# Performance work log

Measured on AMD Instinct MI355X. Metric: run time of the kernel, lower is better.

The kernel has to match this reference:

```python
import jax, jax.numpy as jnp
import numpy as np

N_NODES = 50000
N_EDGES = 800000
IN_C = 128
OUT_C = 128
ALPHA = 0.2  # leaky_relu negative slope (args.egat_alpha)
EDGE_K = 3   # edgefeat width, fixed by W_out in-dim = 3*out_channels


def setup_inputs() -> dict:
    key = jax.random.key(0)
    k = jax.random.split(key, 7)
    h = jax.random.normal(k[0], (N_NODES, IN_C), dtype=jnp.float32)
    edge_index = jax.random.randint(k[1], (2, N_EDGES), 0, N_NODES, dtype=jnp.int64)
    edgefeat = jax.random.uniform(k[2], (N_EDGES, EDGE_K), dtype=jnp.float32)
    # glorot-initialized linear weights (stored as [in, out] for x @ W)
    def glorot(kk, fan_in, fan_out):
        lim = jnp.sqrt(6.0 / (fan_in + fan_out)).astype(jnp.float32)
        return jax.random.uniform(kk, (fan_in, fan_out), jnp.float32, -lim, lim)
    W = glorot(k[3], IN_C, OUT_C)
    a1 = glorot(k[4], OUT_C, 1)
    a2 = glorot(k[5], OUT_C, 1)
    W_out = glorot(k[6], EDGE_K * OUT_C, OUT_C)
    return {"h": h, "edge_index": edge_index, "edgefeat": edgefeat,
            "W": W, "a1": a1, "a2": a2, "W_out": W_out}


def reference(h, edge_index, edgefeat, W, a1, a2, W_out):
    src = edge_index[0]  # j: message source
    dst = edge_index[1]  # i: aggregation target
    n = h.shape[0]

    Wh = h @ W                                   # [N, C]
    s1 = Wh @ a1                                 # [N, 1] alpha_j scores
    s2 = Wh @ a2                                 # [N, 1] alpha_i scores

    # edge_update: leaky_relu(alpha_j + alpha_i) * edge_attr, then edge softmax over dst
    e = s1[src] + s2[dst]                        # [E, 1]
    e = jnp.where(e >= 0, e, ALPHA * e)
    alpha = e * edgefeat                         # [E, 3]
    m = jax.ops.segment_max(alpha, dst, num_segments=n)      # [N, 3]
    m = jnp.where(jnp.isfinite(m), m, 0.0)
    ex = jnp.exp(alpha - m[dst])
    denom = jax.ops.segment_sum(ex, dst, num_segments=n)     # [N, 3]
    att = ex / (denom[dst] + 1e-16)              # [E, 3] (dropout p applied at eval -> identity)

    # message: outer product att[E,3] x x_j[E,C] -> [E, 3C] -> W_out -> [E, C]
    x_j = Wh[src]                                # [E, C]
    msg = (att[:, :, None] * x_j[:, None, :]).reshape(att.shape[0], EDGE_K * Wh.shape[1])
    msg = msg @ W_out                            # [E, C]

    # aggregate: sum at destination nodes
    out = jax.ops.segment_sum(msg, dst, num_segments=n)      # [N, C]
    return out
```

## Files before the change

### kernel.cpp

```cpp
#include <hip/hip_runtime.h>
#include <hip/hip_bf16.h>

#define ALPHA 0.2f
typedef unsigned int uint32;
typedef __attribute__((ext_vector_type(8))) short short8;
typedef __attribute__((ext_vector_type(4))) float f32x4;

static __device__ __forceinline__ unsigned short f2bf(float f) {
    unsigned int u = __float_as_uint(f);
    u += 0x7fffu + ((u >> 16) & 1u);
    return (unsigned short)(u >> 16);
}
static __device__ __forceinline__ uint32 pk2bf(float lo, float hi) {
    return (uint32)f2bf(lo) | ((uint32)f2bf(hi) << 16);
}
static __device__ __forceinline__ float bflo(uint32 u) { return __uint_as_float(u << 16); }
static __device__ __forceinline__ float bfhi(uint32 u) { return __uint_as_float(u & 0xffff0000u); }

__global__ __launch_bounds__(256) void k1_hist_prep(const int* __restrict__ ei,
                                                    int* __restrict__ counts,
                                                    int* __restrict__ eslot, int E,
                                                    const float* __restrict__ W,
                                                    const float* __restrict__ Wout,
                                                    const float* __restrict__ a1,
                                                    const float* __restrict__ a2,
                                                    unsigned short* __restrict__ WT2,
                                                    float* __restrict__ w1f,
                                                    float* __restrict__ w2f, int nbh) {
    __shared__ float Wos[128 * 16];
    const int tid = threadIdx.x;
    if ((int)blockIdx.x < nbh) {
        int e = blockIdx.x * 256 + tid;
        if (e < E) eslot[e] = atomicAdd(&counts[ei[E + e]], 1);
        return;
    }
    int bp = blockIdx.x - nbh;
    if (bp < 24) {
        int s = bp >> 3, nb = bp & 7;
        for (int i = tid; i < 2048; i += 256) {
            int c = i >> 4, q = i & 15;
            Wos[i] = Wout[(size_t)(s * 128 + c) * 128 + nb * 16 + q];
        }
        __syncthreads();
        int j = tid & 127, nh = tid >> 7;
        float acc[8];
#pragma unroll
        for (int p = 0; p < 8; ++p) acc[p] = 0.f;
        for (int c = 0; c < 128; ++c) {
            float w = W[j * 128 + c];
#pragma unroll
            for (int p = 0; p < 8; ++p) acc[p] += w * Wos[c * 16 + nh * 8 + p];
        }
#pragma unroll
        for (int p = 0; p < 8; ++p) {
            int n = nb * 16 + nh * 8 + p;
            WT2[((size_t)s * 128 + n) * 128 + j] = f2bf(acc[p]);
        }
    } else {
        if (tid < 128) {
            float acc1 = 0.f, acc2 = 0.f;
            for (int c = 0; c < 128; ++c) {
                float w = W[tid * 128 + c];
                acc1 += w * a1[c];
                acc2 += w * a2[c];
            }
            w1f[tid] = acc1;
            w2f[tid] = acc2;
        }
    }
}

__global__ __launch_bounds__(256) void k2_mmy_scan(const float* __restrict__ h,
                                                   const unsigned short* __restrict__ WT2,
                                                   const float* __restrict__ w1f,
                                                   const float* __restrict__ w2f,
                                                   unsigned short* __restrict__ Yb,
                                                   float* __restrict__ s1,
                                                   float* __restrict__ s2, int M,
                                                   const int* __restrict__ counts,
                                                   int* __restrict__ rowptr,
                                                   int N, int E, int nbm) {
    __shared__ unsigned short As[64 * 128];
    __shared__ unsigned short Bs[128 * 128];
    __shared__ float ws1[128], ws2[128];
    __shared__ int wsums[4];
    __shared__ int base_s;
    const int tid = threadIdx.x;

    if ((int)blockIdx.x >= nbm) {
        const int bs   = blockIdx.x - nbm;
        const int lane = tid & 63, wv = tid >> 6;
        const int limit = bs * 1024;
        int acc = 0;
        for (int i = tid * 4; i < limit; i += 1024) {
            int4 v = *(const int4*)(counts + i);
            acc += v.x + v.y + v.z + v.w;
        }
#pragma unroll
        for (int off = 32; off > 0; off >>= 1) acc += __shfl_down(acc, off);
        if (lane == 0) wsums[wv] = acc;
        __syncthreads();
        if (tid == 0) base_s = wsums[0] + wsums[1] + wsums[2] + wsums[3];
        __syncthreads();
        int i0 = bs * 1024 + tid * 4;
        int v0 = 0, v1 = 0, v2 = 0, v3 = 0;
        if (i0 + 3 < N) {
            int4 v = *(const int4*)(counts + i0);
            v0 = v.x; v1 = v.y; v2 = v.z; v3 = v.w;
        } else {
            if (i0 + 0 < N) v0 = counts[i0 + 0];
            if (i0 + 1 < N) v1 = counts[i0 + 1];
            if (i0 + 2 < N) v2 = counts[i0 + 2];
            if (i0 + 3 < N) v3 = counts[i0 + 3];
        }
        int tt = v0 + v1 + v2 + v3;
        int incl = tt;
#pragma unroll
        for (int off = 1; off < 64; off <<= 1) {
            int t = __shfl_up(incl, off);
            if (lane >= off) incl += t;
        }
        __syncthreads();
        if (lane == 63) wsums[wv] = incl;
        __syncthreads();
        int woff = 0;
        for (int w2 = 0; w2 < wv; ++w2) woff += wsums[w2];
        int base = base_s + woff + (incl - tt);
        if (i0 + 0 < N) rowptr[i0 + 0] = base;
        if (i0 + 1 < N) rowptr[i0 + 1] = base + v0;
        if (i0 + 2 < N) rowptr[i0 + 2] = base + v0 + v1;
        if (i0 + 3 < N) rowptr[i0 + 3] = base + v0 + v1 + v2;
        if (bs == 0 && tid == 0) rowptr[N] = E;
        return;
    }

    const int lane = tid & 63;
    const int w    = tid >> 6;
    const int row0 = blockIdx.x * 64;

    if (tid < 128) ws1[tid] = w1f[tid];
    else           ws2[tid - 128] = w2f[tid - 128];
    __syncthreads();

    const float4* h4 = (const float4*)h;
    float sp1[4], sp2[4];
#pragma unroll
    for (int m = 0; m < 4; ++m) { sp1[m] = 0.f; sp2[m] = 0.f; }
#pragma unroll
    for (int m = 0; m < 4; ++m) {
        int i = m * 256 + tid;
        int r = i >> 4, g = i & 15;
        int rg = row0 + r;
        float4 va = make_float4(0.f, 0.f, 0.f, 0.f), vb = va;
        if (rg < M) {
            va = h4[(size_t)rg * 32 + g * 2];
            vb = h4[(size_t)rg * 32 + g * 2 + 1];
        }
        float4 wa1 = *(const float4*)(ws1 + g * 8);
        float4 wb1 = *(const float4*)(ws1 + g * 8 + 4);
        float4 wa2 = *(const float4*)(ws2 + g * 8);
        float4 wb2 = *(const float4*)(ws2 + g * 8 + 4);
        sp1[m] += va.x * wa1.x + va.y * wa1.y + va.z * wa1.z + va.w * wa1.w
                + vb.x * wb1.x + vb.y * wb1.y + vb.z * wb1.z + vb.w * wb1.w;
        sp2[m] += va.x * wa2.x + va.y * wa2.y + va.z * wa2.z + va.w * wa2.w
                + vb.x * wb2.x + vb.y * wb2.y + vb.z * wb2.z + vb.w * wb2.w;
        uint4 u;
        u.x = pk2bf(va.x, va.y); u.y = pk2bf(va.z, va.w);
        u.z = pk2bf(vb.x, vb.y); u.w = pk2bf(vb.z, vb.w);
        *(uint4*)(As + r * 128 + ((g ^ (r & 15)) * 8)) = u;
    }
#pragma unroll
    for (int m = 0; m < 4; ++m) {
#pragma unroll
        for (int off = 1; off < 16; off <<= 1) {
            sp1[m] += __shfl_xor(sp1[m], off);
            sp2[m] += __shfl_xor(sp2[m], off);
        }
    }
    if ((tid & 15) == 0) {
#pragma unroll
        for (int m = 0; m < 4; ++m) {
            int rg = row0 + m * 16 + (tid >> 4);
            if (rg < M) { s1[rg] = sp1[m]; s2[rg] = sp2[m]; }
        }
    }

    const int ml   = lane & 15;
    const int quad = lane >> 4;
    for (int ks = 0; ks < 3; ++ks) {
        __syncthreads();
#pragma unroll
        for (int m = 0; m < 8; ++m) {
            int i = m * 256 + tid;
            int n = i >> 4, g = i & 15;
            uint4 v = *(const uint4*)(WT2 + (size_t)ks * 16384 + n * 128 + g * 8);
            *(uint4*)(Bs + n * 128 + ((g ^ (n & 15)) * 8)) = v;
        }
        __syncthreads();

        f32x4 acc[8];
#pragma unroll
        for (int nt = 0; nt < 8; ++nt) acc[nt] = (f32x4){0.f, 0.f, 0.f, 0.f};
#pragma unroll
        for (int kc = 0; kc < 4; ++kc) {
            int gl = ((kc * 4 + quad) ^ ml) * 8;
            short8 af = *(const short8*)(As + (w * 16 + ml) * 128 + gl);
#pragma unroll
            for (int nt = 0; nt < 8; ++nt) {
                short8 bf = *(const short8*)(Bs + (nt * 16 + ml) * 128 + gl);
                acc[nt] = __builtin_amdgcn_mfma_f32_16x16x32_bf16(af, bf, acc[nt], 0, 0, 0);
            }
        }
        __syncthreads();
        unsigned short* Ct = Bs;
        int lrow = w * 16 + quad * 4;
#pragma unroll
        for (int r = 0; r < 4; ++r)
#pragma unroll
            for (int nt = 0; nt < 8; ++nt)
                Ct[(lrow + r) * 136 + nt * 16 + ml] = f2bf(acc[nt][r]);
        __syncthreads();
#pragma unroll
        for (int m = 0; m < 4; ++m) {
            int i = m * 256 + tid;
            int r2 = i >> 4, g = i & 15;
            int rg = row0 + r2;
            uint4 v = *(const uint4*)(Ct + r2 * 136 + g * 8);
            if (rg < M)
                *(uint4*)(Yb + (size_t)rg * 384 + ks * 128 + g * 8) = v;
        }
    }
}

__global__ __launch_bounds__(256) void scatter_kernel(const int* __restrict__ ei,
                                                      const float* __restrict__ ef,
                                                      const float* __restrict__ s1,
                                                      const float* __restrict__ s2,
                                                      const int* __restrict__ rowptr,
                                                      const int* __restrict__ eslot,
                                                      uint2* __restrict__ rec8, int E) {
    int e = blockIdx.x * blockDim.x + threadIdx.x;
    if (e >= E) return;
    int src = ei[e];
    int dst = ei[E + e];
    float s = s1[src] + s2[dst];
    s = (s >= 0.f) ? s : ALPHA * s;
    unsigned short b0 = f2bf(__expf(s * ef[e * 3 + 0]));
    unsigned short b1 = f2bf(__expf(s * ef[e * 3 + 1]));
    unsigned short b2 = f2bf(__expf(s * ef[e * 3 + 2]));
    uint2 rv;
    rv.x = (uint32)src | ((uint32)(b0 & 0x7fffu) << 17);
    rv.y = (uint32)(b1 & 0x7fffu) | ((uint32)(b2 & 0x7fffu) << 15);
    int pos = rowptr[dst] + eslot[e];
    rec8[pos] = rv;
}

__global__ __launch_bounds__(256) void agg_kernel(const uint2* __restrict__ rec8,
                                                  const int* __restrict__ rowptr,
                                                  const uint32* __restrict__ Yu,
                                                  float* __restrict__ out, int N) {
    int node = (blockIdx.x * blockDim.x + threadIdx.x) >> 6;
    int lane = threadIdx.x & 63;
    if (node >= N) return;
    int beg = rowptr[node], end = rowptr[node + 1];

    float d0 = 0.f, d1 = 0.f, d2 = 0.f;
    for (int jb = beg + lane; jb < end; jb += 64) {
        uint2 r = rec8[jb];
        d0 += __uint_as_float((r.x >> 1) & 0x7fff0000u);
        d1 += __uint_as_float((r.y << 16) & 0x7fff0000u);
        d2 += __uint_as_float((r.y << 1) & 0x7fff0000u);
    }
#pragma unroll
    for (int off = 32; off > 0; off >>= 1) {
        d0 += __shfl_xor(d0, off);
        d1 += __shfl_xor(d1, off);
        d2 += __shfl_xor(d2, off);
    }
    float inv0 = 1.f / (d0 + 1e-16f);
    float inv1 = 1.f / (d1 + 1e-16f);
    float inv2 = 1.f / (d2 + 1e-16f);

    float a0 = 0.f, a1 = 0.f;
    int j = beg;
    for (; j + 3 < end; j += 4) {
        uint2 r0 = rec8[j], r1 = rec8[j + 1], r2 = rec8[j + 2], r3 = rec8[j + 3];
        const uint32* p0 = Yu + (size_t)(r0.x & 0x1ffffu) * 192;
        const uint32* p1 = Yu + (size_t)(r1.x & 0x1ffffu) * 192;
        const uint32* p2 = Yu + (size_t)(r2.x & 0x1ffffu) * 192;
        const uint32* p3 = Yu + (size_t)(r3.x & 0x1ffffu) * 192;
        uint32 u00 = p0[lane], u01 = p0[64 + lane], u02 = p0[128 + lane];
        uint32 u10 = p1[lane], u11 = p1[64 + lane], u12 = p1[128 + lane];
        uint32 u20 = p2[lane], u21 = p2[64 + lane], u22 = p2[128 + lane];
        uint32 u30 = p3[lane], u31 = p3[64 + lane], u32 = p3[128 + lane];
        float w00 = __uint_as_float((r0.x >> 1) & 0x7fff0000u) * inv0;
        float w01 = __uint_as_float((r0.y << 16) & 0x7fff0000u) * inv1;
        float w02 = __uint_as_float((r0.y << 1) & 0x7fff0000u) * inv2;
        float w10 = __uint_as_float((r1.x >> 1) & 0x7fff0000u) * inv0;
        float w11 = __uint_as_float((r1.y << 16) & 0x7fff0000u) * inv1;
        float w12 = __uint_as_float((r1.y << 1) & 0x7fff0000u) * inv2;
        float w20 = __uint_as_float((r2.x >> 1) & 0x7fff0000u) * inv0;
        float w21 = __uint_as_float((r2.y << 16) & 0x7fff0000u) * inv1;
        float w22 = __uint_as_float((r2.y << 1) & 0x7fff0000u) * inv2;
        float w30 = __uint_as_float((r3.x >> 1) & 0x7fff0000u) * inv0;
        float w31 = __uint_as_float((r3.y << 16) & 0x7fff0000u) * inv1;
        float w32 = __uint_as_float((r3.y << 1) & 0x7fff0000u) * inv2;
        a0 += w00 * bflo(u00) + w01 * bflo(u01) + w02 * bflo(u02);
        a1 += w00 * bfhi(u00) + w01 * bfhi(u01) + w02 * bfhi(u02);
        a0 += w10 * bflo(u10) + w11 * bflo(u11) + w12 * bflo(u12);
        a1 += w10 * bfhi(u10) + w11 * bfhi(u11) + w12 * bfhi(u12);
        a0 += w20 * bflo(u20) + w21 * bflo(u21) + w22 * bflo(u22);
        a1 += w20 * bfhi(u20) + w21 * bfhi(u21) + w22 * bfhi(u22);
        a0 += w30 * bflo(u30) + w31 * bflo(u31) + w32 * bflo(u32);
        a1 += w30 * bfhi(u30) + w31 * bfhi(u31) + w32 * bfhi(u32);
    }
    for (; j < end; ++j) {
        uint2 r0 = rec8[j];
        const uint32* p0 = Yu + (size_t)(r0.x & 0x1ffffu) * 192;
        uint32 u00 = p0[lane], u01 = p0[64 + lane], u02 = p0[128 + lane];
        float w00 = __uint_as_float((r0.x >> 1) & 0x7fff0000u) * inv0;
        float w01 = __uint_as_float((r0.y << 16) & 0x7fff0000u) * inv1;
        float w02 = __uint_as_float((r0.y << 1) & 0x7fff0000u) * inv2;
        a0 += w00 * bflo(u00) + w01 * bflo(u01) + w02 * bflo(u02);
        a1 += w00 * bfhi(u00) + w01 * bfhi(u01) + w02 * bfhi(u02);
    }
    ((float2*)(out + (size_t)node * 128))[lane] = make_float2(a0, a1);
}

extern "C" void kernel_launch(void* const* d_in, const int* in_sizes, int n_in,
                              void* d_out, int out_size, void* d_ws, size_t ws_size,
                              hipStream_t stream) {
    const float* h    = (const float*)d_in[0];
    const int*   ei   = (const int*)d_in[1];
    const float* ef   = (const float*)d_in[2];
    const float* W    = (const float*)d_in[3];
    const float* a1   = (const float*)d_in[4];
    const float* a2   = (const float*)d_in[5];
    const float* Wout = (const float*)d_in[6];
    float*       out  = (float*)d_out;

    const int N = in_sizes[0] / 128;
    const int E = in_sizes[2] / 3;
    const int nchunk = (N + 1023) / 1024;
    const int nbh    = (E + 255) / 256;
    const int nbm    = (N + 63) / 64;

    uint2* rec8 = (uint2*)d_ws;
    unsigned short* Yb  = (unsigned short*)(rec8 + E);
    unsigned short* WT2 = Yb + (size_t)N * 384;
    float* w1f  = (float*)(WT2 + 3 * 128 * 128);
    float* w2f  = w1f + 128;
    float* s1   = w2f + 128;
    float* s2   = s1 + N;
    int* counts = (int*)(s2 + N);
    int* rowptr = counts + N;
    int* eslot  = rowptr + N + 1;

    (void)hipMemsetAsync(counts, 0, (size_t)N * sizeof(int), stream);

    k1_hist_prep<<<nbh + 25, 256, 0, stream>>>(ei, counts, eslot, E,
                                               W, Wout, a1, a2, WT2, w1f, w2f, nbh);
    k2_mmy_scan<<<nbm + nchunk, 256, 0, stream>>>(h, WT2, w1f, w2f, Yb, s1, s2, N,
                                                  counts, rowptr, N, E, nbm);
    scatter_kernel<<<(E + 255) / 256, 256, 0, stream>>>(ei, ef, s1, s2, rowptr, eslot, rec8, E);
    agg_kernel<<<(N * 64 + 255) / 256, 256, 0, stream>>>(rec8, rowptr, (const uint32*)Yb, out, N);
}
```

Before: 248.7 us.

## Aggregate Wh first then apply W_out in a separate GEMM

The algebra is reordered. Instead of precomputing Y = Wh·W_out per node (three 128-wide slices) and gathering 384 bf16 values per edge, the aggregation now gathers only the 128-wide Wh row per edge. It accumulates three attention-weighted sums per node, normalises them, and stores a bf16 z[N,384]. A new MFMA GEMM kernel then multiplies z by W_out^T to produce the output. This cuts per-edge gather traffic threefold and the first GEMM's work, at the cost of an extra kernel launch, an N×384 intermediate round trip, and extra bf16 rounding of z. The workspace is reordered so counts/eslot alias the z buffer.

Result: faster. 223.5 us (-10.1%).

```diff
diff --git a/kernel.cpp b/kernel.cpp
--- a/kernel.cpp
+++ b/kernel.cpp
@@ -24,10 +24,10 @@
                                                     const float* __restrict__ Wout,
                                                     const float* __restrict__ a1,
                                                     const float* __restrict__ a2,
-                                                    unsigned short* __restrict__ WT2,
+                                                    unsigned short* __restrict__ WBT,
+                                                    unsigned short* __restrict__ WoutT,
                                                     float* __restrict__ w1f,
                                                     float* __restrict__ w2f, int nbh) {
-    __shared__ float Wos[128 * 16];
     const int tid = threadIdx.x;
     if ((int)blockIdx.x < nbh) {
         int e = blockIdx.x * 256 + tid;
@@ -35,27 +35,15 @@
         return;
     }
     int bp = blockIdx.x - nbh;
-    if (bp < 24) {
-        int s = bp >> 3, nb = bp & 7;
-        for (int i = tid; i < 2048; i += 256) {
-            int c = i >> 4, q = i & 15;
-            Wos[i] = Wout[(size_t)(s * 128 + c) * 128 + nb * 16 + q];
-        }
-        __syncthreads();
-        int j = tid & 127, nh = tid >> 7;
-        float acc[8];
-#pragma unroll
-        for (int p = 0; p < 8; ++p) acc[p] = 0.f;
-        for (int c = 0; c < 128; ++c) {
-            float w = W[j * 128 + c];
-#pragma unroll
-            for (int p = 0; p < 8; ++p) acc[p] += w * Wos[c * 16 + nh * 8 + p];
-        }
-#pragma unroll
-        for (int p = 0; p < 8; ++p) {
-            int n = nb * 16 + nh * 8 + p;
-            WT2[((size_t)s * 128 + n) * 128 + j] = f2bf(acc[p]);
-        }
+    if (bp < 8) {
+        for (int n = bp * 16; n < bp * 16 + 16; ++n)
+            for (int c = tid; c < 128; c += 256)
+                WBT[n * 128 + c] = f2bf(W[c * 128 + n]);
+    } else if (bp < 24) {
+        int q = bp - 8;
+        for (int n = q * 8; n < q * 8 + 8; ++n)
+            for (int c = tid; c < 384; c += 256)
+                WoutT[n * 384 + c] = f2bf(Wout[c * 128 + n]);
     } else {
         if (tid < 128) {
             float acc1 = 0.f, acc2 = 0.f;
@@ -71,10 +59,10 @@
 }
 
 __global__ __launch_bounds__(256) void k2_mmy_scan(const float* __restrict__ h,
-                                                   const unsigned short* __restrict__ WT2,
+                                                   const unsigned short* __restrict__ WBT,
                                                    const float* __restrict__ w1f,
                                                    const float* __restrict__ w2f,
-                                                   unsigned short* __restrict__ Yb,
+                                                   unsigned short* __restrict__ Whb,
                                                    float* __restrict__ s1,
                                                    float* __restrict__ s2, int M,
                                                    const int* __restrict__ counts,
@@ -185,50 +173,47 @@
         }
     }
 
+#pragma unroll
+    for (int m = 0; m < 8; ++m) {
+        int i = m * 256 + tid;
+        int n = i >> 4, g = i & 15;
+        uint4 v = *(const uint4*)(WBT + n * 128 + g * 8);
+        *(uint4*)(Bs + n * 128 + ((g ^ (n & 15)) * 8)) = v;
+    }
+    __syncthreads();
+
     const int ml   = lane & 15;
     const int quad = lane >> 4;
-    for (int ks = 0; ks < 3; ++ks) {
-        __syncthreads();
-#pragma unroll
-        for (int m = 0; m < 8; ++m) {
-            int i = m * 256 + tid;
-            int n = i >> 4, g = i & 15;
-            uint4 v = *(const uint4*)(WT2 + (size_t)ks * 16384 + n * 128 + g * 8);
-            *(uint4*)(Bs + n * 128 + ((g ^ (n & 15)) * 8)) = v;
-        }
-        __syncthreads();
-
-        f32x4 acc[8];
-#pragma unroll
-        for (int nt = 0; nt < 8; ++nt) acc[nt] = (f32x4){0.f, 0.f, 0.f, 0.f};
-#pragma unroll
-        for (int kc = 0; kc < 4; ++kc) {
-            int gl = ((kc * 4 + quad) ^ ml) * 8;
-            short8 af = *(const short8*)(As + (w * 16 + ml) * 128 + gl);
-#pragma unroll
-            for (int nt = 0; nt < 8; ++nt) {
-                short8 bf = *(const short8*)(Bs + (nt * 16 + ml) * 128 + gl);
-                acc[nt] = __builtin_amdgcn_mfma_f32_16x16x32_bf16(af, bf, acc[nt], 0, 0, 0);
-            }
-        }
-        __syncthreads();
-        unsigned short* Ct = Bs;
-        int lrow = w * 16 + quad * 4;
-#pragma unroll
-        for (int r = 0; r < 4; ++r)
-#pragma unroll
-            for (int nt = 0; nt < 8; ++nt)
-                Ct[(lrow + r) * 136 + nt * 16 + ml] = f2bf(acc[nt][r]);
-        __syncthreads();
-#pragma unroll
-        for (int m = 0; m < 4; ++m) {
-            int i = m * 256 + tid;
-            int r2 = i >> 4, g = i & 15;
-            int rg = row0 + r2;
-            uint4 v = *(const uint4*)(Ct + r2 * 136 + g * 8);
-            if (rg < M)
-                *(uint4*)(Yb + (size_t)rg * 384 + ks * 128 + g * 8) = v;
-        }
+    f32x4 acc[8];
+#pragma unroll
+    for (int nt = 0; nt < 8; ++nt) acc[nt] = (f32x4){0.f, 0.f, 0.f, 0.f};
+#pragma unroll
+    for (int kc = 0; kc < 4; ++kc) {
+        int gl = ((kc * 4 + quad) ^ ml) * 8;
+        short8 af = *(const short8*)(As + (w * 16 + ml) * 128 + gl);
+#pragma unroll
+        for (int nt = 0; nt < 8; ++nt) {
+            short8 bf = *(const short8*)(Bs + (nt * 16 + ml) * 128 + gl);
+            acc[nt] = __builtin_amdgcn_mfma_f32_16x16x32_bf16(af, bf, acc[nt], 0, 0, 0);
+        }
+    }
+    __syncthreads();
+    unsigned short* Ct = Bs;
+    int lrow = w * 16 + quad * 4;
+#pragma unroll
+    for (int r = 0; r < 4; ++r)
+#pragma unroll
+        for (int nt = 0; nt < 8; ++nt)
+            Ct[(lrow + r) * 136 + nt * 16 + ml] = f2bf(acc[nt][r]);
+    __syncthreads();
+#pragma unroll
+    for (int m = 0; m < 4; ++m) {
+        int i = m * 256 + tid;
+        int r2 = i >> 4, g = i & 15;
+        int rg = row0 + r2;
+        uint4 v = *(const uint4*)(Ct + r2 * 136 + g * 8);
+        if (rg < M)
+            *(uint4*)(Whb + (size_t)rg * 128 + g * 8) = v;
     }
 }
 
@@ -258,73 +243,130 @@
 __global__ __launch_bounds__(256) void agg_kernel(const uint2* __restrict__ rec8,
                                                   const int* __restrict__ rowptr,
                                                   const uint32* __restrict__ Yu,
-                                                  float* __restrict__ out, int N) {
+                                                  uint32* __restrict__ zo, int N) {
     int node = (blockIdx.x * blockDim.x + threadIdx.x) >> 6;
     int lane = threadIdx.x & 63;
     if (node >= N) return;
     int beg = rowptr[node], end = rowptr[node + 1];
 
     float d0 = 0.f, d1 = 0.f, d2 = 0.f;
-    for (int jb = beg + lane; jb < end; jb += 64) {
-        uint2 r = rec8[jb];
-        d0 += __uint_as_float((r.x >> 1) & 0x7fff0000u);
-        d1 += __uint_as_float((r.y << 16) & 0x7fff0000u);
-        d2 += __uint_as_float((r.y << 1) & 0x7fff0000u);
-    }
-#pragma unroll
-    for (int off = 32; off > 0; off >>= 1) {
-        d0 += __shfl_xor(d0, off);
-        d1 += __shfl_xor(d1, off);
-        d2 += __shfl_xor(d2, off);
-    }
-    float inv0 = 1.f / (d0 + 1e-16f);
-    float inv1 = 1.f / (d1 + 1e-16f);
-    float inv2 = 1.f / (d2 + 1e-16f);
-
-    float a0 = 0.f, a1 = 0.f;
+    float z0l = 0.f, z0h = 0.f, z1l = 0.f, z1h = 0.f, z2l = 0.f, z2h = 0.f;
     int j = beg;
     for (; j + 3 < end; j += 4) {
         uint2 r0 = rec8[j], r1 = rec8[j + 1], r2 = rec8[j + 2], r3 = rec8[j + 3];
-        const uint32* p0 = Yu + (size_t)(r0.x & 0x1ffffu) * 192;
-        const uint32* p1 = Yu + (size_t)(r1.x & 0x1ffffu) * 192;
-        const uint32* p2 = Yu + (size_t)(r2.x & 0x1ffffu) * 192;
-        const uint32* p3 = Yu + (size_t)(r3.x & 0x1ffffu) * 192;
-        uint32 u00 = p0[lane], u01 = p0[64 + lane], u02 = p0[128 + lane];
-        uint32 u10 = p1[lane], u11 = p1[64 + lane], u12 = p1[128 + lane];
-        uint32 u20 = p2[lane], u21 = p2[64 + lane], u22 = p2[128 + lane];
-        uint32 u30 = p3[lane], u31 = p3[64 + lane], u32 = p3[128 + lane];
-        float w00 = __uint_as_float((r0.x >> 1) & 0x7fff0000u) * inv0;
-        float w01 = __uint_as_float((r0.y << 16) & 0x7fff0000u) * inv1;
-        float w02 = __uint_as_float((r0.y << 1) & 0x7fff0000u) * inv2;
-        float w10 = __uint_as_float((r1.x >> 1) & 0x7fff0000u) * inv0;
-        float w11 = __uint_as_float((r1.y << 16) & 0x7fff0000u) * inv1;
-        float w12 = __uint_as_float((r1.y << 1) & 0x7fff0000u) * inv2;
-        float w20 = __uint_as_float((r2.x >> 1) & 0x7fff0000u) * inv0;
-        float w21 = __uint_as_float((r2.y << 16) & 0x7fff0000u) * inv1;
-        float w22 = __uint_as_float((r2.y << 1) & 0x7fff0000u) * inv2;
-        float w30 = __uint_as_float((r3.x >> 1) & 0x7fff0000u) * inv0;
-        float w31 = __uint_as_float((r3.y << 16) & 0x7fff0000u) * inv1;
-        float w32 = __uint_as_float((r3.y << 1) & 0x7fff0000u) * inv2;
-        a0 += w00 * bflo(u00) + w01 * bflo(u01) + w02 * bflo(u02);
-        a1 += w00 * bfhi(u00) + w01 * bfhi(u01) + w02 * bfhi(u02);
-        a0 += w10 * bflo(u10) + w11 * bflo(u11) + w12 * bflo(u12);
-        a1 += w10 * bfhi(u10) + w11 * bfhi(u11) + w12 * bfhi(u12);
-        a0 += w20 * bflo(u20) + w21 * bflo(u21) + w22 * bflo(u22);
-        a1 += w20 * bfhi(u20) + w21 * bfhi(u21) + w22 * bfhi(u22);
-        a0 += w30 * bflo(u30) + w31 * bflo(u31) + w32 * bflo(u32);
-        a1 += w30 * bfhi(u30) + w31 * bfhi(u31) + w32 * bfhi(u32);
+        uint32 u0 = Yu[(size_t)(r0.x & 0x1ffffu) * 64 + lane];
+        uint32 u1 = Yu[(size_t)(r1.x & 0x1ffffu) * 64 + lane];
+        uint32 u2 = Yu[(size_t)(r2.x & 0x1ffffu) * 64 + lane];
+        uint32 u3 = Yu[(size_t)(r3.x & 0x1ffffu) * 64 + lane];
+        float w00 = __uint_as_float((r0.x >> 1) & 0x7fff0000u);
+        float w01 = __uint_as_float((r0.y << 16) & 0x7fff0000u);
+        float w02 = __uint_as_float((r0.y << 1) & 0x7fff0000u);
+        float w10 = __uint_as_float((r1.x >> 1) & 0x7fff0000u);
+        float w11 = __uint_as_float((r1.y << 16) & 0x7fff0000u);
+        float w12 = __uint_as_float((r1.y << 1) & 0x7fff0000u);
+        float w20 = __uint_as_float((r2.x >> 1) & 0x7fff0000u);
+        float w21 = __uint_as_float((r2.y << 16) & 0x7fff0000u);
+        float w22 = __uint_as_float((r2.y << 1) & 0x7fff0000u);
+        float w30 = __uint_as_float((r3.x >> 1) & 0x7fff0000u);
+        float w31 = __uint_as_float((r3.y << 16) & 0x7fff0000u);
+        float w32 = __uint_as_float((r3.y << 1) & 0x7fff0000u);
+        d0 += w00 + w10 + w20 + w30;
+        d1 += w01 + w11 + w21 + w31;
+        d2 += w02 + w12 + w22 + w32;
+        float y0l = bflo(u0), y0h = bfhi(u0);
+        float y1l = bflo(u1), y1h = bfhi(u1);
+        float y2l = bflo(u2), y2h = bfhi(u2);
+        float y3l = bflo(u3), y3h = bfhi(u3);
+        z0l += w00 * y0l + w10 * y1l + w20 * y2l + w30 * y3l;
+        z0h += w00 * y0h + w10 * y1h + w20 * y2h + w30 * y3h;
+        z1l += w01 * y0l + w11 * y1l + w21 * y2l + w31 * y3l;
+        z1h += w01 * y0h + w11 * y1h + w21 * y2h + w31 * y3h;
+        z2l += w02 * y0l + w12 * y1l + w22 * y2l + w32 * y3l;
+        z2h += w02 * y0h + w12 * y1h + w22 * y2h + w32 * y3h;
     }
     for (; j < end; ++j) {
         uint2 r0 = rec8[j];
-        const uint32* p0 = Yu + (size_t)(r0.x & 0x1ffffu) * 192;
-        uint32 u00 = p0[lane], u01 = p0[64 + lane], u02 = p0[128 + lane];
-        float w00 = __uint_as_float((r0.x >> 1) & 0x7fff0000u) * inv0;
-        float w01 = __uint_as_float((r0.y << 16) & 0x7fff0000u) * inv1;
-        float w02 = __uint_as_float((r0.y << 1) & 0x7fff0000u) * inv2;
-        a0 += w00 * bflo(u00) + w01 * bflo(u01) + w02 * bflo(u02);
-        a1 += w00 * bfhi(u00) + w01 * bfhi(u01) + w02 * bfhi(u02);
-    }
-    ((float2*)(out + (size_t)node * 128))[lane] = make_float2(a0, a1);
+        uint32 u0 = Yu[(size_t)(r0.x & 0x1ffffu) * 64 + lane];
+        float w00 = __uint_as_float((r0.x >> 1) & 0x7fff0000u);
+        float w01 = __uint_as_float((r0.y << 16) & 0x7fff0000u);
+        float w02 = __uint_as_float((r0.y << 1) & 0x7fff0000u);
+        d0 += w00; d1 += w01; d2 += w02;
+        float y0l = bflo(u0), y0h = bfhi(u0);
+        z0l += w00 * y0l; z0h += w00 * y0h;
+        z1l += w01 * y0l; z1h += w01 * y0h;
+        z2l += w02 * y0l; z2h += w02 * y0h;
+    }
+    float i0 = 1.f / (d0 + 1e-16f);
+    float i1 = 1.f / (d1 + 1e-16f);
+    float i2 = 1.f / (d2 + 1e-16f);
+    size_t zb = (size_t)node * 192;
+    zo[zb + lane]       = pk2bf(z0l * i0, z0h * i0);
+    zo[zb + 64 + lane]  = pk2bf(z1l * i1, z1h * i1);
+    zo[zb + 128 + lane] = pk2bf(z2l * i2, z2h * i2);
+}
+
+__global__ __launch_bounds__(256) void k5_gemm(const unsigned short* __restrict__ z,
+                                               const unsigned short* __restrict__ WoutT,
+                                               float* __restrict__ out, int M) {
+    __shared__ __align__(16) char smem[49152];
+    unsigned short* As = (unsigned short*)smem;
+    unsigned short* Bs = (unsigned short*)(smem + 16384);
+    float* Ct = (float*)smem;
+    const int tid = threadIdx.x;
+    const int lane = tid & 63, w = tid >> 6;
+    const int ml = lane & 15, quad = lane >> 4;
+    const int row0 = blockIdx.x * 64;
+
+    f32x4 acc[8];
+#pragma unroll
+    for (int nt = 0; nt < 8; ++nt) acc[nt] = (f32x4){0.f, 0.f, 0.f, 0.f};
+
+    for (int ks = 0; ks < 3; ++ks) {
+        __syncthreads();
+#pragma unroll
+        for (int m = 0; m < 4; ++m) {
+            int i = m * 256 + tid;
+            int r = i >> 4, g = i & 15;
+            int rg = row0 + r;
+            uint4 v = make_uint4(0u, 0u, 0u, 0u);
+            if (rg < M) v = *(const uint4*)(z + (size_t)rg * 384 + ks * 128 + g * 8);
+            *(uint4*)(As + r * 128 + ((g ^ (r & 15)) * 8)) = v;
+        }
+#pragma unroll
+        for (int m = 0; m < 8; ++m) {
+            int i = m * 256 + tid;
+            int n = i >> 4, g = i & 15;
+            uint4 v = *(const uint4*)(WoutT + n * 384 + ks * 128 + g * 8);
+            *(uint4*)(Bs + n * 128 + ((g ^ (n & 15)) * 8)) = v;
+        }
+        __syncthreads();
+#pragma unroll
+        for (int kc = 0; kc < 4; ++kc) {
+            int gl = ((kc * 4 + quad) ^ ml) * 8;
+            short8 af = *(const short8*)(As + (w * 16 + ml) * 128 + gl);
+#pragma unroll
+            for (int nt = 0; nt < 8; ++nt) {
+                short8 bf = *(const short8*)(Bs + (nt * 16 + ml) * 128 + gl);
+                acc[nt] = __builtin_amdgcn_mfma_f32_16x16x32_bf16(af, bf, acc[nt], 0, 0, 0);
+            }
+        }
+    }
+    __syncthreads();
+    int lrow = w * 16 + quad * 4;
+#pragma unroll
+    for (int r = 0; r < 4; ++r)
+#pragma unroll
+        for (int nt = 0; nt < 8; ++nt)
+            Ct[(lrow + r) * 132 + nt * 16 + ml] = acc[nt][r];
+    __syncthreads();
+#pragma unroll
+    for (int m = 0; m < 8; ++m) {
+        int i = m * 256 + tid;
+        int r2 = i >> 5, g = i & 31;
+        int rg = row0 + r2;
+        if (rg < M)
+            *(float4*)(out + (size_t)rg * 128 + g * 4) = *(const float4*)(Ct + r2 * 132 + g * 4);
+    }
 }
 
 extern "C" void kernel_launch(void* const* d_in, const int* in_sizes, int n_in,
@@ -346,22 +388,26 @@
     const int nbm    = (N + 63) / 64;
 
     uint2* rec8 = (uint2*)d_ws;
-    unsigned short* Yb  = (unsigned short*)(rec8 + E);
-    unsigned short* WT2 = Yb + (size_t)N * 384;
-    float* w1f  = (float*)(WT2 + 3 * 128 * 128);
+    unsigned short* Whb = (unsigned short*)(rec8 + E);
+    unsigned short* WBT = Whb + (size_t)N * 128;
+    unsigned short* WoutT = WBT + 128 * 128;
+    float* w1f  = (float*)(WoutT + 128 * 384);
     float* w2f  = w1f + 128;
     float* s1   = w2f + 128;
     float* s2   = s1 + N;
-    int* counts = (int*)(s2 + N);
-    int* rowptr = counts + N;
-    int* eslot  = rowptr + N + 1;
+    int* rowptr = (int*)(s2 + N);
+    unsigned short* zbuf = (unsigned short*)(rowptr + N + 4);
+    int* counts = (int*)zbuf;
+    int* eslot  = counts + N;
 
     (void)hipMemsetAsync(counts, 0, (size_t)N * sizeof(int), stream);
 
     k1_hist_prep<<<nbh + 25, 256, 0, stream>>>(ei, counts, eslot, E,
-                                               W, Wout, a1, a2, WT2, w1f, w2f, nbh);
-    k2_mmy_scan<<<nbm + nchunk, 256, 0, stream>>>(h, WT2, w1f, w2f, Yb, s1, s2, N,
+                                               W, Wout, a1, a2, WBT, WoutT, w1f, w2f, nbh);
+    k2_mmy_scan<<<nbm + nchunk, 256, 0, stream>>>(h, WBT, w1f, w2f, Whb, s1, s2, N,
                                                   counts, rowptr, N, E, nbm);
     scatter_kernel<<<(E + 255) / 256, 256, 0, stream>>>(ei, ef, s1, s2, rowptr, eslot, rec8, E);
-    agg_kernel<<<(N * 64 + 255) / 256, 256, 0, stream>>>(rec8, rowptr, (const uint32*)Yb, out, N);
-}
+    agg_kernel<<<(N * 64 + 255) / 256, 256, 0, stream>>>(rec8, rowptr, (const uint32*)Whb,
+                                                         (uint32*)zbuf, N);
+    k5_gemm<<<(N + 63) / 64, 256, 0, stream>>>(zbuf, WoutT, out, N);
+}
```
